# Kernel optimization log

Hardware: AMD Instinct MI355X
Metric: run time of the kernel (lower is better)

The kernel has to match this reference:

```python
import jax, jax.numpy as jnp
import numpy as np

S = 2048        # tokens (single prefill sequence)
HID = 3584      # hidden_size
H = 16          # num query heads
KV = 8          # num kv heads
D = 256         # head_dim
WINDOW = 1024   # sliding window size
CAP = 50.0      # logit softcap
SCALE = 256.0 ** -0.5   # query_pre_attn_scalar ** -0.5
THETA = 10000.0


def setup_inputs() -> dict:
    key = jax.random.key(0)
    ks = jax.random.split(key, 5)
    hidden_states = jax.random.normal(ks[0], (S, HID), dtype=jnp.float32)
    positions = jnp.arange(S, dtype=jnp.int32)
    Wq = jax.random.normal(ks[1], (HID, H * D), dtype=jnp.float32) * 0.02
    Wk = jax.random.normal(ks[2], (HID, KV * D), dtype=jnp.float32) * 0.02
    Wv = jax.random.normal(ks[3], (HID, KV * D), dtype=jnp.float32) * 0.02
    Wo = jax.random.normal(ks[4], (H * D, HID), dtype=jnp.float32) * 0.02
    return {"hidden_states": hidden_states, "positions": positions,
            "Wq": Wq, "Wk": Wk, "Wv": Wv, "Wo": Wo}


def _rope_neox(x, positions):
    # x: [S, n_heads, D]; neox-style: rotate halves, full rotary_dim == D
    half = D // 2
    inv_freq = 1.0 / (THETA ** (jnp.arange(0, half, dtype=jnp.float32) * 2.0 / D))
    freqs = positions.astype(jnp.float32)[:, None] * inv_freq[None, :]  # [S, half]
    cos = jnp.cos(freqs)[:, None, :].astype(x.dtype)
    sin = jnp.sin(freqs)[:, None, :].astype(x.dtype)
    x1, x2 = x[..., :half], x[..., half:]
    return jnp.concatenate([x1 * cos - x2 * sin, x2 * cos + x1 * sin], axis=-1)


def reference(hidden_states, positions, Wq, Wk, Wv, Wo):
    # QKV projections (no bias)
    q = (hidden_states @ Wq).reshape(S, H, D)
    k = (hidden_states @ Wk).reshape(S, KV, D)
    v = (hidden_states @ Wv).reshape(S, KV, D)
    q = _rope_neox(q, positions)
    k = _rope_neox(k, positions)
    # grouped-query attention: G query heads per kv head
    G = H // KV
    qg = q.reshape(S, KV, G, D)
    scores = jnp.einsum('qkgd,skd->kgqs', qg, k) * jnp.asarray(SCALE, q.dtype)
    # logit soft-capping
    scores = CAP * jnp.tanh(scores / CAP)
    # causal + sliding-window mask
    i = positions[:, None]
    j = positions[None, :]
    mask = (j <= i) & ((i - j) < WINDOW)   # [S, S]
    neg = jnp.finfo(scores.dtype).min
    scores = jnp.where(mask[None, None, :, :], scores, neg)
    p = jax.nn.softmax(scores, axis=-1)
    attn = jnp.einsum('kgqs,skd->qkgd', p, v).reshape(S, H * D)
    return attn @ Wo
```

## Files before the change

kernel.cpp:

```cpp
#include <hip/hip_runtime.h>
#include <stdint.h>

#define S 2048
#define HID 3584
#define NH 16
#define NKV 8
#define DH 256
#define WINDOW 1024
#define SCALE 0.0625f
#define CAP 50.0f

typedef short s16x8 __attribute__((ext_vector_type(8)));
typedef float f32x4 __attribute__((ext_vector_type(4)));

__device__ __forceinline__ short f2bf(float f) {
  union { float f; uint32_t u; } c; c.f = f;
  uint32_t u = c.u;
  uint32_t r = (u + 0x7FFFu + ((u >> 16) & 1u)) >> 16;
  return (short)r;
}
__device__ __forceinline__ float bf2f(short s) {
  union { uint32_t u; float f; } c;
  c.u = ((uint32_t)(uint16_t)s) << 16;
  return c.f;
}
__device__ __forceinline__ void gll16(const void* g, void* l) {
  __builtin_amdgcn_global_load_lds((const __attribute__((address_space(1))) void*)g,
                                   (__attribute__((address_space(3))) void*)l, 16, 0, 0);
}
#define BAR() asm volatile("s_barrier" ::: "memory")
#define VW6() asm volatile("s_waitcnt vmcnt(6)" ::: "memory")

__global__ void rope_table_kernel(float2* __restrict__ tbl) {
  int idx = blockIdx.x * 256 + threadIdx.x;
  int s = idx >> 7, i = idx & 127;
  float inv = __expf(-(float)i * (9.210340371976184f / 128.0f));
  float fr = (float)s * inv;
  tbl[idx] = make_float2(cosf(fr), sinf(fr));
}

__global__ void conv_hs_kernel(const float* __restrict__ src, short* __restrict__ dst) {
  int gid = blockIdx.x * 256 + threadIdx.x;
  float4 a = *(const float4*)&src[(size_t)gid * 8];
  float4 b = *(const float4*)&src[(size_t)gid * 8 + 4];
  s16x8 o;
  o[0] = f2bf(a.x); o[1] = f2bf(a.y); o[2] = f2bf(a.z); o[3] = f2bf(a.w);
  o[4] = f2bf(b.x); o[5] = f2bf(b.y); o[6] = f2bf(b.z); o[7] = f2bf(b.w);
  *(s16x8*)&dst[(size_t)gid * 8] = o;
}

__global__ __launch_bounds__(256)
void transpose_kernel(const float* __restrict__ src, short* __restrict__ dst,
                      int K, int N)
{
  __shared__ __align__(16) short t[64][76];
  int ntn = N >> 6;
  int tn = blockIdx.x % ntn, tk = blockIdx.x / ntn;
  int tid = threadIdx.x;
  int c = tid & 63, rg = tid >> 6;
  #pragma unroll
  for (int i = 0; i < 4; ++i) {
    int r0 = i * 16 + rg * 4;
    short tmp[4];
    #pragma unroll
    for (int j = 0; j < 4; ++j)
      tmp[j] = f2bf(src[(size_t)(tk * 64 + r0 + j) * N + tn * 64 + c]);
    *(short4*)&t[c][r0] = *(short4*)tmp;
  }
  __syncthreads();
  #pragma unroll
  for (int it = 0; it < 2; ++it) {
    int flat = it * 256 + tid;
    int n = flat >> 3, kc = flat & 7;
    *(s16x8*)&dst[(size_t)(tn * 64 + n) * K + tk * 64 + kc * 8] = *(s16x8*)&t[n][kc * 8];
  }
}

template<int BN, int KS>
__device__ __forceinline__ void gemm_ph(const short* __restrict__ srcA,
                                        const short* __restrict__ srcB,
                                        int tid, int NT,
                                        f32x4 (&acc)[8][BN / 64])
{
  constexpr int NFP = BN / 128;
  constexpr int BTILE = BN * 64;
  __shared__ __align__(16) short Asb[2 * 16384];
  __shared__ __align__(16) short Bsb[2 * BTILE];
  const int wv = tid >> 6, lane = tid & 63;
  const int lr = lane & 15, lk = lane >> 4;
  const int wm_id = wv >> 2, wn_id = wv & 3;
  const int r7 = lr & 7;
  const int abase = (wm_id * 128 + lr) * 64 + ((lk ^ r7) * 8);
  const int bbase = (wn_id * (BN / 4) + lr) * 64 + ((lk ^ r7) * 8);

  s16x8 af[4][2];
  s16x8 bfr[2][NFP][2];

  auto stA = [&](int ts, int r, int b) {
    gll16(srcA + (size_t)ts * 64 + (size_t)(r * 64) * KS,
          Asb + b * 16384 + r * 4096 + wv * 512);
  };
  auto stB = [&](int ts, int q, int b) {
    gll16(srcB + (size_t)ts * 64 + (size_t)(q * 64) * KS,
          Bsb + b * BTILE + q * 4096 + wv * 512);
  };
  auto LDA = [&](int mh, int b) {
    const short* A = Asb + b * 16384;
    #pragma unroll
    for (int mf = 0; mf < 4; ++mf)
      #pragma unroll
      for (int kh = 0; kh < 2; ++kh)
        af[mf][kh] = *(const s16x8*)&A[(abase + (mh * 64 + mf * 16) * 64) ^ (kh * 32)];
  };
  auto LDB = [&](int nh, int b) {
    const short* B = Bsb + b * BTILE;
    #pragma unroll
    for (int nf = 0; nf < NFP; ++nf)
      #pragma unroll
      for (int kh = 0; kh < 2; ++kh)
        bfr[nh][nf][kh] = *(const s16x8*)&B[(bbase + (nh * NFP + nf) * 16 * 64) ^ (kh * 32)];
  };
  auto MMA = [&](int mh, int nh) {
    asm volatile("s_waitcnt lgkmcnt(0)" ::: "memory");
    __builtin_amdgcn_sched_barrier(0);
    __builtin_amdgcn_s_setprio(1);
    #pragma unroll
    for (int mf = 0; mf < 4; ++mf)
      #pragma unroll
      for (int nf = 0; nf < NFP; ++nf) {
        acc[mh * 4 + mf][nh * NFP + nf] =
          __builtin_amdgcn_mfma_f32_16x16x32_bf16(af[mf][0], bfr[nh][nf][0],
                                                  acc[mh * 4 + mf][nh * NFP + nf], 0, 0, 0);
        acc[mh * 4 + mf][nh * NFP + nf] =
          __builtin_amdgcn_mfma_f32_16x16x32_bf16(af[mf][1], bfr[nh][nf][1],
                                                  acc[mh * 4 + mf][nh * NFP + nf], 0, 0, 0);
      }
    __builtin_amdgcn_s_setprio(0);
  };

  #pragma unroll
  for (int r = 0; r < 4; ++r) stA(0, r, 0);
  #pragma unroll
  for (int q = 0; q < BN / 64; ++q) stB(0, q, 0);
  #pragma unroll
  for (int r = 0; r < 4; ++r) stA(1, r, 1);
  stB(1, 0, 1); stB(1, 1, 1);
  asm volatile("s_waitcnt vmcnt(0)" ::: "memory");
  BAR();

  const int NI = NT / 2;
  for (int i = 0; i < NI; ++i) {
    const int T = 2 * i;
    const int t2 = (T + 2 < NT) ? T + 2 : NT - 2;
    const int t3 = (T + 3 < NT) ? T + 3 : NT - 1;
    LDA(0, 0); LDB(0, 0);
    if constexpr (BN == 256) { stB(T + 1, 2, 1); stB(T + 1, 3, 1); }
    BAR(); MMA(0, 0); BAR();
    LDB(1, 0);
    stA(t2, 0, 0); stA(t2, 2, 0);
    BAR(); MMA(0, 1); BAR();
    LDA(1, 0);
    stB(t2, 0, 0); stB(t2, 1, 0);
    BAR(); MMA(1, 0); BAR();
    stA(t2, 1, 0); stA(t2, 3, 0);
    VW6();
    BAR(); MMA(1, 1); BAR();
    LDA(0, 1); LDB(0, 1);
    if constexpr (BN == 256) { stB(t2, 2, 0); stB(t2, 3, 0); }
    BAR(); MMA(0, 0); BAR();
    LDB(1, 1);
    stA(t3, 0, 1); stA(t3, 2, 1);
    BAR(); MMA(0, 1); BAR();
    LDA(1, 1);
    stB(t3, 0, 1); stB(t3, 1, 1);
    BAR(); MMA(1, 0); BAR();
    stA(t3, 1, 1); stA(t3, 3, 1);
    VW6();
    BAR(); MMA(1, 1); BAR();
  }
  asm volatile("s_waitcnt vmcnt(0)" ::: "memory");
}

__global__ __launch_bounds__(512, 2)
void qkv_gemm8_kernel(const short* __restrict__ hsb, const short* __restrict__ Wt,
                      short* __restrict__ qb, short* __restrict__ kbuf,
                      short* __restrict__ vtb)
{
  int bid = blockIdx.x;
  int bm = bid >> 5;
  int bn = (bid & 7) * 4 + ((bid >> 3) & 3);
  int m0 = bm * 256, n0 = bn * 256;
  int tid = threadIdx.x;
  int row8 = tid >> 3;
  int colsw = ((tid & 7) ^ (row8 & 7)) * 8;
  const short* srcA = hsb + (size_t)(m0 + row8) * HID + colsw;
  const short* srcB = Wt + (size_t)(n0 + row8) * HID + colsw;
  f32x4 acc[8][4] = {};
  gemm_ph<256, HID>(srcA, srcB, tid, HID / 64, acc);

  int wv = tid >> 6, lane = tid & 63;
  int lr = lane & 15, lk = lane >> 4;
  int wm = (wv >> 2) * 128, wn = (wv & 3) * 64;
  int region = (n0 < 4096) ? 0 : ((n0 < 6144) ? 1 : 2);
  #pragma unroll
  for (int m = 0; m < 8; ++m) {
    int srow_b = m0 + wm + m * 16 + lk * 4;
    #pragma unroll
    for (int n = 0; n < 4; ++n) {
      int ncol = n0 + wn + n * 16 + lr;
      #pragma unroll
      for (int r = 0; r < 4; ++r) {
        int srow = srow_b + r;
        short bv = f2bf(acc[m][n][r]);
        if (region == 0) {
          int h = ncol >> 8, d = ncol & 255;
          qb[((size_t)h * S + srow) * DH + d] = bv;
        } else if (region == 1) {
          int c = ncol - 4096; int kv = c >> 8, d = c & 255;
          kbuf[((size_t)kv * S + srow) * DH + d] = bv;
        } else {
          int c = ncol - 6144; int kv = c >> 8, d = c & 255;
          vtb[((size_t)kv * DH + d) * S + srow] = bv;
        }
      }
    }
  }
}

__global__ __launch_bounds__(512, 2)
void out_gemm8_kernel(const short* __restrict__ attnb, const short* __restrict__ WtO,
                      float* __restrict__ out)
{
  int bid = blockIdx.x;
  int flat = (bid & 7) * 28 + (bid >> 3);
  int bn = flat >> 3, bm = flat & 7;
  int m0 = bm * 256, n0 = bn * 128;
  int tid = threadIdx.x;
  int row8 = tid >> 3;
  int colsw = ((tid & 7) ^ (row8 & 7)) * 8;
  const short* srcA = attnb + (size_t)(m0 + row8) * 4096 + colsw;
  const short* srcB = WtO + (size_t)(n0 + row8) * 4096 + colsw;
  f32x4 acc[8][2] = {};
  gemm_ph<128, 4096>(srcA, srcB, tid, 4096 / 64, acc);

  int wv = tid >> 6, lane = tid & 63;
  int lr = lane & 15, lk = lane >> 4;
  int wm = (wv >> 2) * 128, wn = (wv & 3) * 32;
  #pragma unroll
  for (int m = 0; m < 8; ++m) {
    int srow_b = m0 + wm + m * 16 + lk * 4;
    #pragma unroll
    for (int n = 0; n < 2; ++n) {
      int ncol = n0 + wn + n * 16 + lr;
      #pragma unroll
      for (int r = 0; r < 4; ++r)
        out[(size_t)(srow_b + r) * HID + ncol] = acc[m][n][r];
    }
  }
}

__global__ void rope_kernel(short* __restrict__ qb, short* __restrict__ kbuf,
                            const float2* __restrict__ tbl)
{
  int gid = blockIdx.x * 256 + threadIdx.x;
  int row = gid >> 4, ch = gid & 15;
  short* base = (row < NH * S) ? (qb + (size_t)row * DH)
                               : (kbuf + (size_t)(row - NH * S) * DH);
  int s = row & (S - 1);
  int i0 = ch * 8;
  s16x8 x1 = *(s16x8*)(base + i0);
  s16x8 x2 = *(s16x8*)(base + 128 + i0);
  s16x8 y1, y2;
  #pragma unroll
  for (int j = 0; j < 8; ++j) {
    float2 cs = tbl[s * 128 + i0 + j];
    float a = bf2f(x1[j]), b = bf2f(x2[j]);
    y1[j] = f2bf(a * cs.x - b * cs.y);
    y2[j] = f2bf(b * cs.x + a * cs.y);
  }
  *(s16x8*)(base + i0) = y1;
  *(s16x8*)(base + 128 + i0) = y2;
}

__global__ __launch_bounds__(512)
void attn_kernel(const short* __restrict__ qb, const short* __restrict__ kbuf,
                 const short* __restrict__ vtb, short* __restrict__ attnb)
{
  __shared__ __align__(16) short Klds[2][64][256];
  __shared__ __align__(16) short Vlds[2][256][72];
  __shared__ __align__(16) short Plds[8][16][72];
  int bid = blockIdx.x;
  int qt = 31 - (bid >> 4), h = bid & 15;
  int kv = h >> 1;
  int q0 = qt * 64;
  int tid = threadIdx.x;
  int w = tid >> 6, lane = tid & 63;
  int g = w >> 2, wsub = w & 3;
  int gtid = tid & 255;
  int lr = lane & 15, lk = lane >> 4;
  int qrow_base = q0 + wsub * 16;
  s16x8 qf[8];
  const short* qrow = qb + ((size_t)h * S + (qrow_base + lr)) * DH;
  #pragma unroll
  for (int kb = 0; kb < 8; ++kb)
    qf[kb] = *(const s16x8*)(qrow + kb * 32 + lk * 8);
  f32x4 acc_o[16] = {};
  float l_r[4] = {0.0f, 0.0f, 0.0f, 0.0f};
  int tlo = (q0 >= WINDOW - 1) ? ((q0 - (WINDOW - 1)) >> 6) : 0;
  int thi = q0 >> 6;
  const short* kbase = kbuf + (size_t)kv * S * DH;
  const short* vbase = vtb + (size_t)kv * DH * S;

  s16x8 kpf[8], vpf[8];
  auto loadRegs = [&](int t) {
    int k0 = t * 64;
    #pragma unroll
    for (int it = 0; it < 8; ++it) {
      int flat = it * 256 + gtid;
      int r = flat >> 5, cg = flat & 31;
      kpf[it] = *(const s16x8*)(kbase + (size_t)(k0 + r) * DH + cg * 8);
    }
    #pragma unroll
    for (int it = 0; it < 8; ++it) {
      int flat = it * 256 + gtid;
      int r = flat >> 3, cg = flat & 7;
      vpf[it] = *(const s16x8*)(vbase + (size_t)r * S + k0 + cg * 8);
    }
  };
  auto writeLds = [&]() {
    #pragma unroll
    for (int it = 0; it < 8; ++it) {
      int flat = it * 256 + gtid;
      int r = flat >> 5, cg = flat & 31;
      *(s16x8*)&Klds[g][r][(cg ^ (r & 7)) * 8] = kpf[it];
    }
    #pragma unroll
    for (int it = 0; it < 8; ++it) {
      int flat = it * 256 + gtid;
      int r = flat >> 3, cg = flat & 7;
      *(s16x8*)&Vlds[g][r][(cg ^ (r & 7)) * 8] = vpf[it];
    }
  };

  int tg0 = tlo + g;
  int n_all = thi - tlo + 1;
  int jmax = (n_all + 1) >> 1;
  if (tg0 <= thi) loadRegs(tg0);
  for (int j = 0; j < jmax; ++j) {
    int t = tg0 + 2 * j;
    bool active = (t <= thi);
    if (active) writeLds();
    __syncthreads();
    if (active && t + 2 <= thi) loadRegs(t + 2);
    if (active) {
      int k0 = t * 64;
      f32x4 sc4[4] = {};
      __builtin_amdgcn_s_setprio(1);
      #pragma unroll
      for (int kb = 0; kb < 8; ++kb)
        #pragma unroll
        for (int ni = 0; ni < 4; ++ni) {
          int row = ni * 16 + lr;
          s16x8 b = *(const s16x8*)&Klds[g][row][(((kb << 2) | lk) ^ (row & 7)) * 8];
          sc4[ni] = __builtin_amdgcn_mfma_f32_16x16x32_bf16(qf[kb], b, sc4[ni], 0, 0, 0);
        }
      __builtin_amdgcn_s_setprio(0);
      bool interior = (k0 + 63 <= qrow_base) && (qrow_base + 15 - k0 < WINDOW);
      #pragma unroll
      for (int ni = 0; ni < 4; ++ni)
        #pragma unroll
        for (int r = 0; r < 4; ++r) {
          float raw = sc4[ni][r];
          float u = fabsf(raw) * (2.0f * SCALE / CAP);
          float e = __expf(-u);
          float th = (1.0f - e) / (1.0f + e);
          float z = CAP * copysignf(th, raw) - CAP;
          if (!interior) {
            int qg = qrow_base + lk * 4 + r;
            int kg = k0 + ni * 16 + lr;
            bool valid = (kg <= qg) && (qg - kg < WINDOW);
            z = valid ? z : -1e30f;
          }
          float p = __expf(z);
          sc4[ni][r] = p;
          l_r[r] += p;
        }
      #pragma unroll
      for (int ni = 0; ni < 4; ++ni)
        #pragma unroll
        for (int r = 0; r < 4; ++r)
          Plds[w][lk * 4 + r][ni * 16 + lr] = f2bf(sc4[ni][r]);
      s16x8 pa0 = *(const s16x8*)&Plds[w][lr][lk * 8];
      s16x8 pa1 = *(const s16x8*)&Plds[w][lr][32 + lk * 8];
      __builtin_amdgcn_s_setprio(1);
      #pragma unroll
      for (int df = 0; df < 16; ++df) {
        int row = df * 16 + lr;
        s16x8 b0 = *(const s16x8*)&Vlds[g][row][((lk ^ (row & 7)) * 8)];
        s16x8 b1 = *(const s16x8*)&Vlds[g][row][(((4 + lk) ^ (row & 7)) * 8)];
        acc_o[df] = __builtin_amdgcn_mfma_f32_16x16x32_bf16(pa0, b0, acc_o[df], 0, 0, 0);
        acc_o[df] = __builtin_amdgcn_mfma_f32_16x16x32_bf16(pa1, b1, acc_o[df], 0, 0, 0);
      }
      __builtin_amdgcn_s_setprio(0);
    }
    __syncthreads();
  }
  float lsum[4];
  #pragma unroll
  for (int r = 0; r < 4; ++r) {
    float v = l_r[r];
    #pragma unroll
    for (int off = 1; off < 16; off <<= 1)
      v += __shfl_xor(v, off, 64);
    lsum[r] = v;
  }
  float* comb = (float*)&Klds[0][0][0];
  float* lcomb = (float*)&Vlds[0][0][0];
  if (g == 1) {
    #pragma unroll
    for (int df = 0; df < 16; ++df)
      #pragma unroll
      for (int r = 0; r < 4; ++r)
        comb[(size_t)(wsub * 16 + lk * 4 + r) * 256 + df * 16 + lr] = acc_o[df][r];
    if (lr == 0)
      #pragma unroll
      for (int r = 0; r < 4; ++r)
        lcomb[wsub * 16 + lk * 4 + r] = lsum[r];
  }
  __syncthreads();
  if (g == 0) {
    #pragma unroll
    for (int r = 0; r < 4; ++r) {
      int rowi = wsub * 16 + lk * 4 + r;
      float lt = lsum[r] + lcomb[rowi];
      float inv = 1.0f / lt;
      int srow = q0 + rowi;
      #pragma unroll
      for (int df = 0; df < 16; ++df) {
        float o = acc_o[df][r] + comb[(size_t)rowi * 256 + df * 16 + lr];
        attnb[(size_t)srow * (NH * DH) + h * DH + df * 16 + lr] = f2bf(o * inv);
      }
    }
  }
}

extern "C" void kernel_launch(void* const* d_in, const int* in_sizes, int n_in,
                              void* d_out, int out_size, void* d_ws, size_t ws_size,
                              hipStream_t stream) {
  const float* hs = (const float*)d_in[0];
  const float* Wq = (const float*)d_in[2];
  const float* Wk = (const float*)d_in[3];
  const float* Wv = (const float*)d_in[4];
  const float* Wo = (const float*)d_in[5];
  float* out = (float*)d_out;
  char* ws = (char*)d_ws;
  size_t off = 0;
  float2* tbl  = (float2*)(ws + off); off += 2097152;
  short* qb    = (short*)(ws + off);  off += 16777216;
  short* kbuf  = (short*)(ws + off);  off += 8388608;
  short* vtb   = (short*)(ws + off);  off += 8388608;
  short* attnb = (short*)(ws + off);  off += 16777216;
  short* hsb   = (short*)(ws + off);  off += 14680064;
  short* Wt    = (short*)(ws + off);  off += 58720256;
  short* WtO   = (short*)(ws + off);  off += 29360128;

  hipLaunchKernelGGL(rope_table_kernel, dim3(1024), dim3(256), 0, stream, tbl);
  hipLaunchKernelGGL(conv_hs_kernel, dim3(3584), dim3(256), 0, stream, hs, hsb);
  hipLaunchKernelGGL(transpose_kernel, dim3(64 * 56), dim3(256), 0, stream,
                     Wq, Wt, HID, 4096);
  hipLaunchKernelGGL(transpose_kernel, dim3(32 * 56), dim3(256), 0, stream,
                     Wk, Wt + (size_t)4096 * HID, HID, 2048);
  hipLaunchKernelGGL(transpose_kernel, dim3(32 * 56), dim3(256), 0, stream,
                     Wv, Wt + (size_t)6144 * HID, HID, 2048);
  hipLaunchKernelGGL(transpose_kernel, dim3(56 * 64), dim3(256), 0, stream,
                     Wo, WtO, 4096, HID);
  hipLaunchKernelGGL(qkv_gemm8_kernel, dim3(256), dim3(512), 0, stream,
                     hsb, Wt, qb, kbuf, vtb);
  hipLaunchKernelGGL(rope_kernel, dim3(3072), dim3(256), 0, stream, qb, kbuf, tbl);
  hipLaunchKernelGGL(attn_kernel, dim3(512), dim3(512), 0, stream,
                     qb, kbuf, vtb, attnb);
  hipLaunchKernelGGL(out_gemm8_kernel, dim3(224), dim3(512), 0, stream,
                     attnb, WtO, out);
}
```

Baseline: 394.6 us.

## Replace pipelined 8-wave GEMMs with simple single-buffer GEMMs and merge transposes

New measurement: 377.6 us. 1.05x faster.

```diff
diff --git a/kernel.cpp b/kernel.cpp
--- a/kernel.cpp
+++ b/kernel.cpp
@@ -28,8 +28,6 @@
   __builtin_amdgcn_global_load_lds((const __attribute__((address_space(1))) void*)g,
                                    (__attribute__((address_space(3))) void*)l, 16, 0, 0);
 }
-#define BAR() asm volatile("s_barrier" ::: "memory")
-#define VW6() asm volatile("s_waitcnt vmcnt(6)" ::: "memory")
 
 __global__ void rope_table_kernel(float2* __restrict__ tbl) {
   int idx = blockIdx.x * 256 + threadIdx.x;
@@ -50,12 +48,19 @@
 }
 
 __global__ __launch_bounds__(256)
-void transpose_kernel(const float* __restrict__ src, short* __restrict__ dst,
-                      int K, int N)
+void transpose_all_kernel(const float* __restrict__ Wq, const float* __restrict__ Wk,
+                          const float* __restrict__ Wv, const float* __restrict__ Wo,
+                          short* __restrict__ Wt, short* __restrict__ WtO)
 {
   __shared__ __align__(16) short t[64][76];
+  int b = blockIdx.x;
+  const float* src; short* dst; int K, N, lb;
+  if (b < 3584)      { src = Wq; dst = Wt;                       K = HID;  N = 4096; lb = b; }
+  else if (b < 5376) { src = Wk; dst = Wt + (size_t)4096 * HID;  K = HID;  N = 2048; lb = b - 3584; }
+  else if (b < 7168) { src = Wv; dst = Wt + (size_t)6144 * HID;  K = HID;  N = 2048; lb = b - 5376; }
+  else               { src = Wo; dst = WtO;                      K = 4096; N = HID;  lb = b - 7168; }
   int ntn = N >> 6;
-  int tn = blockIdx.x % ntn, tk = blockIdx.x / ntn;
+  int tn = lb % ntn, tk = lb / ntn;
   int tid = threadIdx.x;
   int c = tid & 63, rg = tid >> 6;
   #pragma unroll
@@ -76,131 +81,67 @@
   }
 }
 
-template<int BN, int KS>
-__device__ __forceinline__ void gemm_ph(const short* __restrict__ srcA,
-                                        const short* __restrict__ srcB,
-                                        int tid, int NT,
-                                        f32x4 (&acc)[8][BN / 64])
+__global__ __launch_bounds__(256, 2)
+void qkv_gemm_kernel(const short* __restrict__ hsb, const short* __restrict__ Wt,
+                     short* __restrict__ qb, short* __restrict__ kbuf,
+                     short* __restrict__ vtb)
 {
-  constexpr int NFP = BN / 128;
-  constexpr int BTILE = BN * 64;
-  __shared__ __align__(16) short Asb[2 * 16384];
-  __shared__ __align__(16) short Bsb[2 * BTILE];
-  const int wv = tid >> 6, lane = tid & 63;
-  const int lr = lane & 15, lk = lane >> 4;
-  const int wm_id = wv >> 2, wn_id = wv & 3;
-  const int r7 = lr & 7;
-  const int abase = (wm_id * 128 + lr) * 64 + ((lk ^ r7) * 8);
-  const int bbase = (wn_id * (BN / 4) + lr) * 64 + ((lk ^ r7) * 8);
-
-  s16x8 af[4][2];
-  s16x8 bfr[2][NFP][2];
-
-  auto stA = [&](int ts, int r, int b) {
-    gll16(srcA + (size_t)ts * 64 + (size_t)(r * 64) * KS,
-          Asb + b * 16384 + r * 4096 + wv * 512);
-  };
-  auto stB = [&](int ts, int q, int b) {
-    gll16(srcB + (size_t)ts * 64 + (size_t)(q * 64) * KS,
-          Bsb + b * BTILE + q * 4096 + wv * 512);
-  };
-  auto LDA = [&](int mh, int b) {
-    const short* A = Asb + b * 16384;
-    #pragma unroll
-    for (int mf = 0; mf < 4; ++mf)
-      #pragma unroll
-      for (int kh = 0; kh < 2; ++kh)
-        af[mf][kh] = *(const s16x8*)&A[(abase + (mh * 64 + mf * 16) * 64) ^ (kh * 32)];
-  };
-  auto LDB = [&](int nh, int b) {
-    const short* B = Bsb + b * BTILE;
-    #pragma unroll
-    for (int nf = 0; nf < NFP; ++nf)
-      #pragma unroll
-      for (int kh = 0; kh < 2; ++kh)
-        bfr[nh][nf][kh] = *(const s16x8*)&B[(bbase + (nh * NFP + nf) * 16 * 64) ^ (kh * 32)];
-  };
-  auto MMA = [&](int mh, int nh) {
-    asm volatile("s_waitcnt lgkmcnt(0)" ::: "memory");
-    __builtin_amdgcn_sched_barrier(0);
-    __builtin_amdgcn_s_setprio(1);
-    #pragma unroll
-    for (int mf = 0; mf < 4; ++mf)
-      #pragma unroll
-      for (int nf = 0; nf < NFP; ++nf) {
-        acc[mh * 4 + mf][nh * NFP + nf] =
-          __builtin_amdgcn_mfma_f32_16x16x32_bf16(af[mf][0], bfr[nh][nf][0],
-                                                  acc[mh * 4 + mf][nh * NFP + nf], 0, 0, 0);
-        acc[mh * 4 + mf][nh * NFP + nf] =
-          __builtin_amdgcn_mfma_f32_16x16x32_bf16(af[mf][1], bfr[nh][nf][1],
-                                                  acc[mh * 4 + mf][nh * NFP + nf], 0, 0, 0);
-      }
-    __builtin_amdgcn_s_setprio(0);
-  };
-
-  #pragma unroll
-  for (int r = 0; r < 4; ++r) stA(0, r, 0);
-  #pragma unroll
-  for (int q = 0; q < BN / 64; ++q) stB(0, q, 0);
-  #pragma unroll
-  for (int r = 0; r < 4; ++r) stA(1, r, 1);
-  stB(1, 0, 1); stB(1, 1, 1);
-  asm volatile("s_waitcnt vmcnt(0)" ::: "memory");
-  BAR();
-
-  const int NI = NT / 2;
-  for (int i = 0; i < NI; ++i) {
-    const int T = 2 * i;
-    const int t2 = (T + 2 < NT) ? T + 2 : NT - 2;
-    const int t3 = (T + 3 < NT) ? T + 3 : NT - 1;
-    LDA(0, 0); LDB(0, 0);
-    if constexpr (BN == 256) { stB(T + 1, 2, 1); stB(T + 1, 3, 1); }
-    BAR(); MMA(0, 0); BAR();
-    LDB(1, 0);
-    stA(t2, 0, 0); stA(t2, 2, 0);
-    BAR(); MMA(0, 1); BAR();
-    LDA(1, 0);
-    stB(t2, 0, 0); stB(t2, 1, 0);
-    BAR(); MMA(1, 0); BAR();
-    stA(t2, 1, 0); stA(t2, 3, 0);
-    VW6();
-    BAR(); MMA(1, 1); BAR();
-    LDA(0, 1); LDB(0, 1);
-    if constexpr (BN == 256) { stB(t2, 2, 0); stB(t2, 3, 0); }
-    BAR(); MMA(0, 0); BAR();
-    LDB(1, 1);
-    stA(t3, 0, 1); stA(t3, 2, 1);
-    BAR(); MMA(0, 1); BAR();
-    LDA(1, 1);
-    stB(t3, 0, 1); stB(t3, 1, 1);
-    BAR(); MMA(1, 0); BAR();
-    stA(t3, 1, 1); stA(t3, 3, 1);
-    VW6();
-    BAR(); MMA(1, 1); BAR();
-  }
-  asm volatile("s_waitcnt vmcnt(0)" ::: "memory");
-}
-
-__global__ __launch_bounds__(512, 2)
-void qkv_gemm8_kernel(const short* __restrict__ hsb, const short* __restrict__ Wt,
-                      short* __restrict__ qb, short* __restrict__ kbuf,
-                      short* __restrict__ vtb)
-{
+  __shared__ __align__(16) short Asb[256 * 64];
+  __shared__ __align__(16) short Bsb[128 * 64];
   int bid = blockIdx.x;
-  int bm = bid >> 5;
-  int bn = (bid & 7) * 4 + ((bid >> 3) & 3);
-  int m0 = bm * 256, n0 = bn * 256;
-  int tid = threadIdx.x;
+  int i = bid >> 3;
+  int bm = i & 7;
+  int bn = (bid & 7) * 8 + (i >> 3);
+  int m0 = bm * 256, n0 = bn * 128;
+  int tid = threadIdx.x, w = tid >> 6, lane = tid & 63;
+  int lr = lane & 15, lk = lane >> 4;
+  int wm = (w >> 1) * 128, wn = (w & 1) * 64;
+  int r7 = lr & 7;
+  int abase = (wm + lr) * 64 + ((lk ^ r7) * 8);
+  int bbase = (wn + lr) * 64 + ((lk ^ r7) * 8);
   int row8 = tid >> 3;
   int colsw = ((tid & 7) ^ (row8 & 7)) * 8;
   const short* srcA = hsb + (size_t)(m0 + row8) * HID + colsw;
   const short* srcB = Wt + (size_t)(n0 + row8) * HID + colsw;
   f32x4 acc[8][4] = {};
-  gemm_ph<256, HID>(srcA, srcB, tid, HID / 64, acc);
-
-  int wv = tid >> 6, lane = tid & 63;
-  int lr = lane & 15, lk = lane >> 4;
-  int wm = (wv >> 2) * 128, wn = (wv & 3) * 64;
+  for (int t = 0; t < HID / 64; ++t) {
+    const short* sa = srcA + t * 64;
+    const short* sb = srcB + t * 64;
+    #pragma unroll
+    for (int r = 0; r < 8; ++r)
+      gll16(sa + (size_t)(r * 32) * HID, Asb + r * 2048 + w * 512);
+    #pragma unroll
+    for (int r = 0; r < 4; ++r)
+      gll16(sb + (size_t)(r * 32) * HID, Bsb + r * 2048 + w * 512);
+    __syncthreads();
+    s16x8 bf[4][2];
+    #pragma unroll
+    for (int nf = 0; nf < 4; ++nf)
+      #pragma unroll
+      for (int kh = 0; kh < 2; ++kh)
+        bf[nf][kh] = *(const s16x8*)&Bsb[(bbase + nf * 16 * 64) ^ (kh * 32)];
+    #pragma unroll
+    for (int mh = 0; mh < 2; ++mh) {
+      s16x8 af[4][2];
+      #pragma unroll
+      for (int mf = 0; mf < 4; ++mf)
+        #pragma unroll
+        for (int kh = 0; kh < 2; ++kh)
+          af[mf][kh] = *(const s16x8*)&Asb[(abase + (mh * 64 + mf * 16) * 64) ^ (kh * 32)];
+      __builtin_amdgcn_s_setprio(1);
+      #pragma unroll
+      for (int mf = 0; mf < 4; ++mf)
+        #pragma unroll
+        for (int nf = 0; nf < 4; ++nf) {
+          acc[mh * 4 + mf][nf] = __builtin_amdgcn_mfma_f32_16x16x32_bf16(
+              af[mf][0], bf[nf][0], acc[mh * 4 + mf][nf], 0, 0, 0);
+          acc[mh * 4 + mf][nf] = __builtin_amdgcn_mfma_f32_16x16x32_bf16(
+              af[mf][1], bf[nf][1], acc[mh * 4 + mf][nf], 0, 0, 0);
+        }
+      __builtin_amdgcn_s_setprio(0);
+    }
+    __syncthreads();
+  }
   int region = (n0 < 4096) ? 0 : ((n0 < 6144) ? 1 : 2);
   #pragma unroll
   for (int m = 0; m < 8; ++m) {
@@ -227,34 +168,67 @@
   }
 }
 
-__global__ __launch_bounds__(512, 2)
-void out_gemm8_kernel(const short* __restrict__ attnb, const short* __restrict__ WtO,
-                      float* __restrict__ out)
+__global__ __launch_bounds__(256)
+void out_gemm_kernel(const short* __restrict__ attnb, const short* __restrict__ WtO,
+                     float* __restrict__ out)
 {
+  __shared__ __align__(16) short Asb[128 * 64];
+  __shared__ __align__(16) short Bsb[128 * 64];
   int bid = blockIdx.x;
-  int flat = (bid & 7) * 28 + (bid >> 3);
-  int bn = flat >> 3, bm = flat & 7;
-  int m0 = bm * 256, n0 = bn * 128;
-  int tid = threadIdx.x;
+  int flat = (bid & 7) * 56 + (bid >> 3);
+  int bn = flat >> 4, bm = flat & 15;
+  int m0 = bm * 128, n0 = bn * 128;
+  int tid = threadIdx.x, w = tid >> 6, lane = tid & 63;
+  int lr = lane & 15, lk = lane >> 4;
+  int wm = (w >> 1) * 64, wn = (w & 1) * 64;
+  int r7 = lr & 7;
+  int abase = (wm + lr) * 64 + ((lk ^ r7) * 8);
+  int bbase = (wn + lr) * 64 + ((lk ^ r7) * 8);
   int row8 = tid >> 3;
   int colsw = ((tid & 7) ^ (row8 & 7)) * 8;
   const short* srcA = attnb + (size_t)(m0 + row8) * 4096 + colsw;
   const short* srcB = WtO + (size_t)(n0 + row8) * 4096 + colsw;
-  f32x4 acc[8][2] = {};
-  gemm_ph<128, 4096>(srcA, srcB, tid, 4096 / 64, acc);
-
-  int wv = tid >> 6, lane = tid & 63;
-  int lr = lane & 15, lk = lane >> 4;
-  int wm = (wv >> 2) * 128, wn = (wv & 3) * 32;
-  #pragma unroll
-  for (int m = 0; m < 8; ++m) {
-    int srow_b = m0 + wm + m * 16 + lk * 4;
-    #pragma unroll
-    for (int n = 0; n < 2; ++n) {
-      int ncol = n0 + wn + n * 16 + lr;
+  f32x4 acc[4][4] = {};
+  for (int t = 0; t < 4096 / 64; ++t) {
+    const short* sa = srcA + t * 64;
+    const short* sb = srcB + t * 64;
+    #pragma unroll
+    for (int r = 0; r < 4; ++r)
+      gll16(sa + (size_t)(r * 32) * 4096, Asb + r * 2048 + w * 512);
+    #pragma unroll
+    for (int r = 0; r < 4; ++r)
+      gll16(sb + (size_t)(r * 32) * 4096, Bsb + r * 2048 + w * 512);
+    __syncthreads();
+    s16x8 af[4][2], bf[4][2];
+    #pragma unroll
+    for (int f = 0; f < 4; ++f)
+      #pragma unroll
+      for (int kh = 0; kh < 2; ++kh) {
+        af[f][kh] = *(const s16x8*)&Asb[(abase + f * 16 * 64) ^ (kh * 32)];
+        bf[f][kh] = *(const s16x8*)&Bsb[(bbase + f * 16 * 64) ^ (kh * 32)];
+      }
+    __builtin_amdgcn_s_setprio(1);
+    #pragma unroll
+    for (int mf = 0; mf < 4; ++mf)
+      #pragma unroll
+      for (int nf = 0; nf < 4; ++nf) {
+        acc[mf][nf] = __builtin_amdgcn_mfma_f32_16x16x32_bf16(
+            af[mf][0], bf[nf][0], acc[mf][nf], 0, 0, 0);
+        acc[mf][nf] = __builtin_amdgcn_mfma_f32_16x16x32_bf16(
+            af[mf][1], bf[nf][1], acc[mf][nf], 0, 0, 0);
+      }
+    __builtin_amdgcn_s_setprio(0);
+    __syncthreads();
+  }
+  #pragma unroll
+  for (int mf = 0; mf < 4; ++mf) {
+    int srow_b = m0 + wm + mf * 16 + lk * 4;
+    #pragma unroll
+    for (int nf = 0; nf < 4; ++nf) {
+      int ncol = n0 + wn + nf * 16 + lr;
       #pragma unroll
       for (int r = 0; r < 4; ++r)
-        out[(size_t)(srow_b + r) * HID + ncol] = acc[m][n][r];
+        out[(size_t)(srow_b + r) * HID + ncol] = acc[mf][nf][r];
     }
   }
 }
@@ -287,7 +261,7 @@
                  const short* __restrict__ vtb, short* __restrict__ attnb)
 {
   __shared__ __align__(16) short Klds[2][64][256];
-  __shared__ __align__(16) short Vlds[2][256][72];
+  __shared__ __align__(16) short Vlds[2][256][64];
   __shared__ __align__(16) short Plds[8][16][72];
   int bid = blockIdx.x;
   int qt = 31 - (bid >> 4), h = bid & 15;
@@ -371,17 +345,15 @@
         #pragma unroll
         for (int r = 0; r < 4; ++r) {
           float raw = sc4[ni][r];
-          float u = fabsf(raw) * (2.0f * SCALE / CAP);
-          float e = __expf(-u);
-          float th = (1.0f - e) / (1.0f + e);
-          float z = CAP * copysignf(th, raw) - CAP;
+          float e = __expf(-fabsf(raw) * (2.0f * SCALE / CAP));
+          float wgt = raw > 0.0f ? e : 1.0f;
+          float p = __expf(-2.0f * CAP * __fdividef(wgt, 1.0f + e));
           if (!interior) {
             int qg = qrow_base + lk * 4 + r;
             int kg = k0 + ni * 16 + lr;
             bool valid = (kg <= qg) && (qg - kg < WINDOW);
-            z = valid ? z : -1e30f;
+            p = valid ? p : 0.0f;
           }
-          float p = __expf(z);
           sc4[ni][r] = p;
           l_r[r] += p;
         }
@@ -466,19 +438,13 @@
 
   hipLaunchKernelGGL(rope_table_kernel, dim3(1024), dim3(256), 0, stream, tbl);
   hipLaunchKernelGGL(conv_hs_kernel, dim3(3584), dim3(256), 0, stream, hs, hsb);
-  hipLaunchKernelGGL(transpose_kernel, dim3(64 * 56), dim3(256), 0, stream,
-                     Wq, Wt, HID, 4096);
-  hipLaunchKernelGGL(transpose_kernel, dim3(32 * 56), dim3(256), 0, stream,
-                     Wk, Wt + (size_t)4096 * HID, HID, 2048);
-  hipLaunchKernelGGL(transpose_kernel, dim3(32 * 56), dim3(256), 0, stream,
-                     Wv, Wt + (size_t)6144 * HID, HID, 2048);
-  hipLaunchKernelGGL(transpose_kernel, dim3(56 * 64), dim3(256), 0, stream,
-                     Wo, WtO, 4096, HID);
-  hipLaunchKernelGGL(qkv_gemm8_kernel, dim3(256), dim3(512), 0, stream,
+  hipLaunchKernelGGL(transpose_all_kernel, dim3(10752), dim3(256), 0, stream,
+                     Wq, Wk, Wv, Wo, Wt, WtO);
+  hipLaunchKernelGGL(qkv_gemm_kernel, dim3(512), dim3(256), 0, stream,
                      hsb, Wt, qb, kbuf, vtb);
   hipLaunchKernelGGL(rope_kernel, dim3(3072), dim3(256), 0, stream, qb, kbuf, tbl);
   hipLaunchKernelGGL(attn_kernel, dim3(512), dim3(512), 0, stream,
                      qb, kbuf, vtb, attnb);
-  hipLaunchKernelGGL(out_gemm8_kernel, dim3(224), dim3(512), 0, stream,
+  hipLaunchKernelGGL(out_gemm_kernel, dim3(448), dim3(256), 0, stream,
                      attnb, WtO, out);
 }
```
